# Optimization experiments

Measured on AMD Instinct MI355X. Metric: run time of the kernel, lower is better.

## Reference

```python
import jax, jax.numpy as jnp
import numpy as np

H = 12  # num_heads

def setup_inputs() -> dict:
    key = jax.random.key(0)
    ks = jax.random.split(key, 6)
    B, L, D = 2, 2048, 768
    x = jax.random.normal(ks[0], (B, L, D), dtype=jnp.float32)
    token_sizes = jax.random.uniform(ks[1], (B, L), dtype=jnp.float32)
    attn_mask = jnp.triu(jnp.ones((L, L), dtype=bool), k=1)
    key_padding_mask = jnp.zeros((B, L), dtype=bool)
    qkv_w = jax.random.normal(ks[2], (3 * D, D), dtype=jnp.float32) * (D ** -0.5)
    qkv_b = jax.random.normal(ks[3], (3 * D,), dtype=jnp.float32) * 0.02
    proj_w = jax.random.normal(ks[4], (D, D), dtype=jnp.float32) * (D ** -0.5)
    proj_b = jax.random.normal(ks[5], (D,), dtype=jnp.float32) * 0.02
    return {"x": x, "token_sizes": token_sizes, "attn_mask": attn_mask,
            "key_padding_mask": key_padding_mask, "qkv_w": qkv_w, "qkv_b": qkv_b,
            "proj_w": proj_w, "proj_b": proj_b}

def reference(x, token_sizes, attn_mask, key_padding_mask, qkv_w, qkv_b, proj_w, proj_b):
    B, L, D = x.shape
    hd = D // H
    scale = hd ** -0.5
    qkv = (x @ qkv_w.T + qkv_b).reshape(B, L, 3, H, hd)
    qkv = jnp.transpose(qkv, (2, 0, 3, 1, 4))  # [3, B, H, L, hd]
    q, k, v = qkv[0], qkv[1], qkv[2]
    logits = jnp.einsum('bhqd,bhkd->bhqk', q, k) * scale  # [B,H,L,L]
    neg = jnp.finfo(logits.dtype).min
    logits = jnp.where(attn_mask[None, None, :, :], neg, logits)
    logits = jnp.where(key_padding_mask[:, None, None, :], neg, logits)
    logits = logits + jnp.log(jnp.clip(token_sizes, 1e-8))[:, None, None, :]
    attn = jax.nn.softmax(logits, axis=-1)
    out = jnp.einsum('bhqk,bhkd->bhqd', attn, v)
    out = jnp.transpose(out, (0, 2, 1, 3)).reshape(B, L, D)
    out = out @ proj_w.T + proj_b
    k_merge = k.mean(axis=1)  # [B, L, hd]
    return (out, k_merge)
```

## Files before the change

### kernel.cpp

```cpp
#include <hip/hip_runtime.h>
#include <hip/hip_bf16.h>

typedef unsigned short u16;
typedef __bf16 bf16x8 __attribute__((ext_vector_type(8)));
typedef float f32x4 __attribute__((ext_vector_type(4)));

#define QSCALE (0.125f * 1.44269504088896340736f)

__device__ __forceinline__ u16 f2bf(float f) {
    __hip_bfloat16 h = __float2bfloat16(f);
    return __builtin_bit_cast(u16, h);
}
__device__ __forceinline__ float bf2f(u16 u) {
    unsigned int x = ((unsigned int)u) << 16;
    return __builtin_bit_cast(float, x);
}
__device__ __forceinline__ bf16x8 ld_bf8(const u16* p) {
    uint4 u = *reinterpret_cast<const uint4*>(p);
    return __builtin_bit_cast(bf16x8, u);
}
__device__ __forceinline__ bf16x8 pack8f(f32x4 a, f32x4 b) {
    union { bf16x8 v; u16 u[8]; } r;
    #pragma unroll
    for (int i = 0; i < 4; i++) { r.u[i] = f2bf(a[i]); r.u[4+i] = f2bf(b[i]); }
    return r.v;
}
__device__ __forceinline__ bf16x8 pack8u(ushort4 a, ushort4 b) {
    union { bf16x8 v; ushort4 u[2]; } r;
    r.u[0] = a; r.u[1] = b;
    return r.v;
}

#define GLOAD_LDS16(g, l) __builtin_amdgcn_global_load_lds( \
    (const __attribute__((address_space(1))) unsigned int*)(g), \
    (__attribute__((address_space(3))) unsigned int*)(l), 16, 0, 0)

__global__ __launch_bounds__(256) void prep_kernel(
    const float* __restrict__ x, const float* __restrict__ qkvw,
    const float* __restrict__ projw, const float* __restrict__ ts,
    const unsigned char* __restrict__ kpm,
    u16* __restrict__ Xb, u16* __restrict__ Wq, u16* __restrict__ Wp,
    float* __restrict__ tsw, int* __restrict__ qcount)
{
    int i = blockIdx.x * 256 + threadIdx.x;
    if (i == 0) *qcount = 0;
    const int XC4 = 4096 * 768 / 4;
    const int WQ4 = 2304 * 768 / 4;
    const int WP4 = 768 * 768 / 4;
    const float* src = nullptr; u16* dst = nullptr;
    if (i < XC4) { src = x; dst = Xb; }
    else {
        i -= XC4;
        if (i < WQ4) { src = qkvw; dst = Wq; }
        else {
            i -= WQ4;
            if (i < WP4) { src = projw; dst = Wp; }
            else {
                i -= WP4;
                if (i < 1024) {
                    float4 t = *(const float4*)(ts + i*4);
                    uchar4 k = *(const uchar4*)(kpm + i*4);
                    float4 r;
                    r.x = k.x ? 0.f : fmaxf(t.x, 1e-8f);
                    r.y = k.y ? 0.f : fmaxf(t.y, 1e-8f);
                    r.z = k.z ? 0.f : fmaxf(t.z, 1e-8f);
                    r.w = k.w ? 0.f : fmaxf(t.w, 1e-8f);
                    *(float4*)(tsw + i*4) = r;
                }
                return;
            }
        }
    }
    float4 v = *(const float4*)(src + i*4);
    ushort4 o;
    o.x = f2bf(v.x); o.y = f2bf(v.y); o.z = f2bf(v.z); o.w = f2bf(v.w);
    *(ushort4*)(dst + i*4) = o;
}

template<int EPI>
__global__ __launch_bounds__(256) void gemm_bt(
    const u16* __restrict__ A, const u16* __restrict__ Bm,
    const float* __restrict__ bias,
    u16* __restrict__ Qb, u16* __restrict__ Kb, u16* __restrict__ Vt,
    float* __restrict__ outp)
{
    __shared__ u16 As[2][128 * 32];
    __shared__ u16 Bs[2][128 * 32];
    const int K = 768;
    const int tid = threadIdx.x;
    const int m0 = blockIdx.y * 128;
    const int n0 = blockIdx.x * 128;
    const int w = tid >> 6, lane = tid & 63;
    const int wr = (w >> 1) * 64, wc = (w & 1) * 64;
    const int g = lane >> 4, l16 = lane & 15;

    const int srow = lane >> 2;
    const int scol = (lane & 3) * 8;
    const u16* gA0 = A  + (size_t)(m0 + w*32      + srow) * K + scol;
    const u16* gA1 = A  + (size_t)(m0 + w*32 + 16 + srow) * K + scol;
    const u16* gB0 = Bm + (size_t)(n0 + w*32      + srow) * K + scol;
    const u16* gB1 = Bm + (size_t)(n0 + w*32 + 16 + srow) * K + scol;

#define GSTAGE(buf, kk) do { \
    GLOAD_LDS16(gA0 + (kk), &As[buf][(w*32     ) * 32]); \
    GLOAD_LDS16(gA1 + (kk), &As[buf][(w*32 + 16) * 32]); \
    GLOAD_LDS16(gB0 + (kk), &Bs[buf][(w*32     ) * 32]); \
    GLOAD_LDS16(gB1 + (kk), &Bs[buf][(w*32 + 16) * 32]); } while (0)

    f32x4 acc[4][4] = {};
    GSTAGE(0, 0);
    __syncthreads();
    for (int k0 = 0; k0 < K; k0 += 32) {
        const int cur = (k0 >> 5) & 1;
        if (k0 + 32 < K) GSTAGE(cur ^ 1, k0 + 32);
        bf16x8 af[4], bfr[4];
        #pragma unroll
        for (int i = 0; i < 4; i++) af[i]  = ld_bf8(&As[cur][(wr + i*16 + l16)*32 + g*8]);
        #pragma unroll
        for (int j = 0; j < 4; j++) bfr[j] = ld_bf8(&Bs[cur][(wc + j*16 + l16)*32 + g*8]);
        #pragma unroll
        for (int i = 0; i < 4; i++)
            #pragma unroll
            for (int j = 0; j < 4; j++)
                acc[i][j] = __builtin_amdgcn_mfma_f32_16x16x32_bf16(af[i], bfr[j], acc[i][j], 0, 0, 0);
        __syncthreads();
    }
#undef GSTAGE

    #pragma unroll
    for (int j = 0; j < 4; j++) {
        const int n = n0 + wc + j*16 + l16;
        const float bs = bias[n];
        #pragma unroll
        for (int i = 0; i < 4; i++) {
            #pragma unroll
            for (int r = 0; r < 4; r++) {
                const int m = m0 + wr + i*16 + g*4 + r;
                float v = acc[i][j][r] + bs;
                if (EPI == 0) {
                    int b = m >> 11, l = m & 2047;
                    unsigned int which = (unsigned int)n / 768u;
                    int rem = n - (int)which * 768;
                    int h = rem >> 6, d = rem & 63;
                    int bh = b * 12 + h;
                    if (which == 0)      Qb[((size_t)bh*2048 + l)*64 + d] = f2bf(v * QSCALE);
                    else if (which == 1) Kb[((size_t)bh*2048 + l)*64 + d] = f2bf(v);
                    else                 Vt[((size_t)bh*64 + d)*2048 + l] = f2bf(v);
                } else {
                    outp[(size_t)m * 768 + n] = v;
                }
            }
        }
    }
}

__global__ __launch_bounds__(256, 2) void attn_kernel(
    const u16* __restrict__ Q, const u16* __restrict__ Kb,
    const u16* __restrict__ Vt, const float* __restrict__ tsw,
    u16* __restrict__ O, int* __restrict__ qcount)
{
    __shared__ u16 Ks[2][64 * 64];
    __shared__ u16 Vs[2][64 * 64];
    __shared__ int s_item;
    const int tid = threadIdx.x;
    const int w = tid >> 6, lane = tid & 63;
    const int g = lane >> 4, l16 = lane & 15;
    const int sw = l16 & 7;
    const int srow = lane >> 3;
    const int sslot = (lane & 7) ^ srow;

    bf16x8 ones;
    { union { bf16x8 v; u16 u[8]; } t;
      #pragma unroll
      for (int i = 0; i < 8; i++) t.u[i] = 0x3F80;
      ones = t.v; }

    for (;;) {
        if (tid == 0) s_item = atomicAdd(qcount, 1);
        __syncthreads();
        const int item = s_item;
        if (item >= 768) return;
        const int qt = 31 - (item / 24);
        const int bh = item - (item / 24) * 24;
        const int b = bh / 12, h = bh - b * 12;
        const int q0 = qt * 64 + w * 16;
        const int nkt = qt + 1;

        const u16* Qp = Q + ((size_t)bh * 2048 + q0) * 64;
        const u16* Kp = Kb + (size_t)bh * 2048 * 64;
        const u16* Vp = Vt + (size_t)bh * 64 * 2048;
        const float* tw = tsw + b * 2048;

        const u16* gK0 = Kp + (size_t)(w*16 +     srow) * 64   + sslot * 8;
        const u16* gK1 = Kp + (size_t)(w*16 + 8 + srow) * 64   + sslot * 8;
        const u16* gV0 = Vp + (size_t)(w*16 +     srow) * 2048 + sslot * 8;
        const u16* gV1 = Vp + (size_t)(w*16 + 8 + srow) * 2048 + sslot * 8;

#define ASTAGE(buf, kk) do { \
    GLOAD_LDS16(gK0 + (size_t)(kk) * 64, &Ks[buf][(w*16    ) * 64]); \
    GLOAD_LDS16(gK1 + (size_t)(kk) * 64, &Ks[buf][(w*16 + 8) * 64]); \
    GLOAD_LDS16(gV0 + (kk),              &Vs[buf][(w*16    ) * 64]); \
    GLOAD_LDS16(gV1 + (kk),              &Vs[buf][(w*16 + 8) * 64]); } while (0)

        const bf16x8 qf0 = ld_bf8(Qp + l16 * 64 + g * 8);
        const bf16x8 qf1 = ld_bf8(Qp + l16 * 64 + 32 + g * 8);

        f32x4 o[4] = {};
        f32x4 lpacc = {};
        float m = -1e30f;
        const int qmy = q0 + l16;

        ASTAGE(0, 0);
        __syncthreads();

        for (int kt = 0; kt < nkt; kt++) {
            const int cur = kt & 1;
            const int k0 = kt * 64;
            if (kt + 1 < nkt) ASTAGE(cur ^ 1, k0 + 64);

            f32x4 twv[4];
            #pragma unroll
            for (int t = 0; t < 4; t++)
                twv[t] = *(const f32x4*)(tw + k0 + t*16 + 4*g);

            const int ko0 = 8 * (g ^ sw);
            f32x4 s[4];
            #pragma unroll
            for (int t = 0; t < 4; t++) {
                const u16* kb = &Ks[cur][(t*16 + l16) * 64];
                bf16x8 kf0 = ld_bf8(kb + ko0);
                bf16x8 kf1 = ld_bf8(kb + (ko0 ^ 32));
                f32x4 z = {};
                z = __builtin_amdgcn_mfma_f32_16x16x32_bf16(kf0, qf0, z, 0, 0, 0);
                z = __builtin_amdgcn_mfma_f32_16x16x32_bf16(kf1, qf1, z, 0, 0, 0);
                s[t] = z;
            }
            if (kt == qt) {
                #pragma unroll
                for (int t = 0; t < 4; t++)
                    #pragma unroll
                    for (int r = 0; r < 4; r++) {
                        const int key = k0 + t*16 + 4*g + r;
                        if (key > qmy) s[t][r] = -1e30f;
                    }
            }
            float pmax = -1e30f;
            #pragma unroll
            for (int t = 0; t < 4; t++)
                #pragma unroll
                for (int r = 0; r < 4; r++)
                    pmax = fmaxf(pmax, s[t][r]);
            pmax = fmaxf(pmax, __shfl_xor(pmax, 16));
            pmax = fmaxf(pmax, __shfl_xor(pmax, 32));
            if (!__all(pmax <= m + 8.f)) {
                const float mn = fmaxf(m, pmax);
                const float sc = __builtin_amdgcn_exp2f(m - mn);
                m = mn;
                #pragma unroll
                for (int r = 0; r < 4; r++) {
                    const float scr = __shfl(sc, (lane & 48) + 4*g + r);
                    o[0][r] *= scr; o[1][r] *= scr; o[2][r] *= scr; o[3][r] *= scr;
                    lpacc[r] *= scr;
                }
            }
            #pragma unroll
            for (int t = 0; t < 4; t++)
                #pragma unroll
                for (int r = 0; r < 4; r++)
                    s[t][r] = __builtin_amdgcn_exp2f(s[t][r] - m) * twv[t][r];
            const bf16x8 pa01 = pack8f(s[0], s[1]);
            const bf16x8 pa23 = pack8f(s[2], s[3]);
            lpacc = __builtin_amdgcn_mfma_f32_16x16x32_bf16(pa01, ones, lpacc, 0, 0, 0);
            lpacc = __builtin_amdgcn_mfma_f32_16x16x32_bf16(pa23, ones, lpacc, 0, 0, 0);
            const int gh = g >> 1, gl = 4 * (g & 1);
            #pragma unroll
            for (int j = 0; j < 4; j++) {
                const u16* vb = &Vs[cur][(j*16 + l16) * 64];
                ushort4 va0 = *(const ushort4*)(vb + (((0 + gh) ^ sw) << 3) + gl);
                ushort4 va1 = *(const ushort4*)(vb + (((2 + gh) ^ sw) << 3) + gl);
                ushort4 va2 = *(const ushort4*)(vb + (((4 + gh) ^ sw) << 3) + gl);
                ushort4 va3 = *(const ushort4*)(vb + (((6 + gh) ^ sw) << 3) + gl);
                o[j] = __builtin_amdgcn_mfma_f32_16x16x32_bf16(pa01, pack8u(va0, va1), o[j], 0, 0, 0);
                o[j] = __builtin_amdgcn_mfma_f32_16x16x32_bf16(pa23, pack8u(va2, va3), o[j], 0, 0, 0);
            }
            __syncthreads();
        }
#undef ASTAGE

        float rlr[4];
        #pragma unroll
        for (int r = 0; r < 4; r++) rlr[r] = 1.f / lpacc[r];
        #pragma unroll
        for (int j = 0; j < 4; j++)
            #pragma unroll
            for (int r = 0; r < 4; r++) {
                const int q = q0 + 4*g + r;
                O[((size_t)b*2048 + q)*768 + h*64 + j*16 + l16] = f2bf(o[j][r] * rlr[r]);
            }
    }
}

__global__ __launch_bounds__(256) void kmerge_kernel(
    const u16* __restrict__ Kb, float* __restrict__ out)
{
    const int idx = blockIdx.x * 256 + threadIdx.x;
    const int d4 = (idx & 15) * 4;
    const int l = (idx >> 4) & 2047;
    const int b = idx >> 15;
    float4 acc = {0.f, 0.f, 0.f, 0.f};
    #pragma unroll
    for (int h = 0; h < 12; h++) {
        ushort4 v = *(const ushort4*)&Kb[(((size_t)(b*12 + h))*2048 + l)*64 + d4];
        acc.x += bf2f(v.x); acc.y += bf2f(v.y);
        acc.z += bf2f(v.z); acc.w += bf2f(v.w);
    }
    const float s = 1.f / 12.f;
    float4 r = {acc.x * s, acc.y * s, acc.z * s, acc.w * s};
    *(float4*)&out[(((size_t)b*2048 + l))*64 + d4] = r;
}

extern "C" void kernel_launch(void* const* d_in, const int* in_sizes, int n_in,
                              void* d_out, int out_size, void* d_ws, size_t ws_size,
                              hipStream_t stream)
{
    const float* x     = (const float*)d_in[0];
    const float* ts    = (const float*)d_in[1];
    const unsigned char* kpm = (const unsigned char*)d_in[3];
    const float* qkvw  = (const float*)d_in[4];
    const float* qkvb  = (const float*)d_in[5];
    const float* projw = (const float*)d_in[6];
    const float* projb = (const float*)d_in[7];
    float* out = (float*)d_out;

    char* ws = (char*)d_ws;
    u16* Xb = (u16*)ws;  ws += (size_t)4096 * 768 * 2;
    u16* Wq = (u16*)ws;  ws += (size_t)2304 * 768 * 2;
    u16* Wp = (u16*)ws;  ws += (size_t)768 * 768 * 2;
    u16* Qb = (u16*)ws;  ws += (size_t)24 * 2048 * 64 * 2;
    u16* Kb = (u16*)ws;  ws += (size_t)24 * 2048 * 64 * 2;
    u16* Vt = (u16*)ws;  ws += (size_t)24 * 2048 * 64 * 2;
    u16* Ob = (u16*)ws;  ws += (size_t)4096 * 768 * 2;
    float* tsw = (float*)ws;  ws += (size_t)2 * 2048 * 4;
    int* qcount = (int*)ws;

    const int prep4 = (4096*768 + 2304*768 + 768*768) / 4 + 1024;
    prep_kernel<<<(prep4 + 255) / 256, 256, 0, stream>>>(
        x, qkvw, projw, ts, kpm, Xb, Wq, Wp, tsw, qcount);

    gemm_bt<0><<<dim3(18, 32), 256, 0, stream>>>(Xb, Wq, qkvb, Qb, Kb, Vt, nullptr);

    attn_kernel<<<dim3(640), 256, 0, stream>>>(Qb, Kb, Vt, tsw, Ob, qcount);

    kmerge_kernel<<<(2*2048*16) / 256, 256, 0, stream>>>(Kb, out + 3145728);

    gemm_bt<1><<<dim3(6, 32), 256, 0, stream>>>(Ob, Wp, projb, nullptr, nullptr, nullptr, out);
}
```

Baseline: 118.8 us.

## Fold token-size weights into V and row-sum MFMA, swizzle GEMM blocks, hoist LDS loads

Token-size weights are now multiplied into V in the QKV GEMM epilogue. The softmax denominator uses a bf16 weight vector as the MFMA B operand, which removes the per-element weight multiply and the fp32 weight loads in the attention inner loop. GEMM workgroup indices are remapped in groups of eight to improve L2 locality. K and V fragments are loaded from LDS before the score MFMAs so the loads have more time to land, and the attention grid drops from 640 to 512 persistent blocks. The risks are bf16 rounding of the weights in both V and the denominator, and higher register pressure from hoisting the fragments.

```diff
diff --git a/kernel.cpp b/kernel.cpp
--- a/kernel.cpp
+++ b/kernel.cpp
@@ -40,7 +40,7 @@
     const float* __restrict__ projw, const float* __restrict__ ts,
     const unsigned char* __restrict__ kpm,
     u16* __restrict__ Xb, u16* __restrict__ Wq, u16* __restrict__ Wp,
-    float* __restrict__ tsw, int* __restrict__ qcount)
+    float* __restrict__ tsw, u16* __restrict__ tbf, int* __restrict__ qcount)
 {
     int i = blockIdx.x * 256 + threadIdx.x;
     if (i == 0) *qcount = 0;
@@ -66,6 +66,10 @@
                     r.z = k.z ? 0.f : fmaxf(t.z, 1e-8f);
                     r.w = k.w ? 0.f : fmaxf(t.w, 1e-8f);
                     *(float4*)(tsw + i*4) = r;
+                    ushort4 o;
+                    o.x = f2bf(r.x); o.y = f2bf(r.y);
+                    o.z = f2bf(r.z); o.w = f2bf(r.w);
+                    *(ushort4*)(tbf + i*4) = o;
                 }
                 return;
             }
@@ -80,7 +84,7 @@
 template<int EPI>
 __global__ __launch_bounds__(256) void gemm_bt(
     const u16* __restrict__ A, const u16* __restrict__ Bm,
-    const float* __restrict__ bias,
+    const float* __restrict__ bias, const float* __restrict__ tsw,
     u16* __restrict__ Qb, u16* __restrict__ Kb, u16* __restrict__ Vt,
     float* __restrict__ outp)
 {
@@ -88,8 +92,12 @@
     __shared__ u16 Bs[2][128 * 32];
     const int K = 768;
     const int tid = threadIdx.x;
-    const int m0 = blockIdx.y * 128;
-    const int n0 = blockIdx.x * 128;
+    const int nwg = gridDim.x * gridDim.y;
+    const int flat = blockIdx.y * gridDim.x + blockIdx.x;
+    const int per = nwg >> 3;
+    const int swz = (flat & 7) * per + (flat >> 3);
+    const int m0 = (swz / gridDim.x) * 128;
+    const int n0 = (swz % gridDim.x) * 128;
     const int w = tid >> 6, lane = tid & 63;
     const int wr = (w >> 1) * 64, wc = (w & 1) * 64;
     const int g = lane >> 4, l16 = lane & 15;
@@ -145,7 +153,7 @@
                     int bh = b * 12 + h;
                     if (which == 0)      Qb[((size_t)bh*2048 + l)*64 + d] = f2bf(v * QSCALE);
                     else if (which == 1) Kb[((size_t)bh*2048 + l)*64 + d] = f2bf(v);
-                    else                 Vt[((size_t)bh*64 + d)*2048 + l] = f2bf(v);
+                    else                 Vt[((size_t)bh*64 + d)*2048 + l] = f2bf(v * tsw[b*2048 + l]);
                 } else {
                     outp[(size_t)m * 768 + n] = v;
                 }
@@ -156,7 +164,7 @@
 
 __global__ __launch_bounds__(256, 2) void attn_kernel(
     const u16* __restrict__ Q, const u16* __restrict__ Kb,
-    const u16* __restrict__ Vt, const float* __restrict__ tsw,
+    const u16* __restrict__ Vt, const u16* __restrict__ tbf,
     u16* __restrict__ O, int* __restrict__ qcount)
 {
     __shared__ u16 Ks[2][64 * 64];
@@ -168,12 +176,6 @@
     const int sw = l16 & 7;
     const int srow = lane >> 3;
     const int sslot = (lane & 7) ^ srow;
-
-    bf16x8 ones;
-    { union { bf16x8 v; u16 u[8]; } t;
-      #pragma unroll
-      for (int i = 0; i < 8; i++) t.u[i] = 0x3F80;
-      ones = t.v; }
 
     for (;;) {
         if (tid == 0) s_item = atomicAdd(qcount, 1);
@@ -189,7 +191,7 @@
         const u16* Qp = Q + ((size_t)bh * 2048 + q0) * 64;
         const u16* Kp = Kb + (size_t)bh * 2048 * 64;
         const u16* Vp = Vt + (size_t)bh * 64 * 2048;
-        const float* tw = tsw + b * 2048;
+        const u16* tb = tbf + b * 2048;
 
         const u16* gK0 = Kp + (size_t)(w*16 +     srow) * 64   + sslot * 8;
         const u16* gK1 = Kp + (size_t)(w*16 + 8 + srow) * 64   + sslot * 8;
@@ -216,23 +218,40 @@
         for (int kt = 0; kt < nkt; kt++) {
             const int cur = kt & 1;
             const int k0 = kt * 64;
+
+            const u16* tp = tb + k0 + 4*g;
+            ushort4 t0 = *(const ushort4*)(tp);
+            ushort4 t1 = *(const ushort4*)(tp + 16);
+            ushort4 t2 = *(const ushort4*)(tp + 32);
+            ushort4 t3 = *(const ushort4*)(tp + 48);
+
             if (kt + 1 < nkt) ASTAGE(cur ^ 1, k0 + 64);
 
-            f32x4 twv[4];
-            #pragma unroll
-            for (int t = 0; t < 4; t++)
-                twv[t] = *(const f32x4*)(tw + k0 + t*16 + 4*g);
-
             const int ko0 = 8 * (g ^ sw);
-            f32x4 s[4];
+            bf16x8 kf[4][2];
             #pragma unroll
             for (int t = 0; t < 4; t++) {
                 const u16* kb = &Ks[cur][(t*16 + l16) * 64];
-                bf16x8 kf0 = ld_bf8(kb + ko0);
-                bf16x8 kf1 = ld_bf8(kb + (ko0 ^ 32));
+                kf[t][0] = ld_bf8(kb + ko0);
+                kf[t][1] = ld_bf8(kb + (ko0 ^ 32));
+            }
+            const int gh = g >> 1, gl = 4 * (g & 1);
+            ushort4 va[4][4];
+            #pragma unroll
+            for (int j = 0; j < 4; j++) {
+                const u16* vb = &Vs[cur][(j*16 + l16) * 64];
+                va[j][0] = *(const ushort4*)(vb + (((0 + gh) ^ sw) << 3) + gl);
+                va[j][1] = *(const ushort4*)(vb + (((2 + gh) ^ sw) << 3) + gl);
+                va[j][2] = *(const ushort4*)(vb + (((4 + gh) ^ sw) << 3) + gl);
+                va[j][3] = *(const ushort4*)(vb + (((6 + gh) ^ sw) << 3) + gl);
+            }
+
+            f32x4 s[4];
+            #pragma unroll
+            for (int t = 0; t < 4; t++) {
                 f32x4 z = {};
-                z = __builtin_amdgcn_mfma_f32_16x16x32_bf16(kf0, qf0, z, 0, 0, 0);
-                z = __builtin_amdgcn_mfma_f32_16x16x32_bf16(kf1, qf1, z, 0, 0, 0);
+                z = __builtin_amdgcn_mfma_f32_16x16x32_bf16(kf[t][0], qf0, z, 0, 0, 0);
+                z = __builtin_amdgcn_mfma_f32_16x16x32_bf16(kf[t][1], qf1, z, 0, 0, 0);
                 s[t] = z;
             }
             if (kt == qt) {
@@ -267,21 +286,15 @@
             for (int t = 0; t < 4; t++)
                 #pragma unroll
                 for (int r = 0; r < 4; r++)
-                    s[t][r] = __builtin_amdgcn_exp2f(s[t][r] - m) * twv[t][r];
+                    s[t][r] = __builtin_amdgcn_exp2f(s[t][r] - m);
             const bf16x8 pa01 = pack8f(s[0], s[1]);
             const bf16x8 pa23 = pack8f(s[2], s[3]);
-            lpacc = __builtin_amdgcn_mfma_f32_16x16x32_bf16(pa01, ones, lpacc, 0, 0, 0);
-            lpacc = __builtin_amdgcn_mfma_f32_16x16x32_bf16(pa23, ones, lpacc, 0, 0, 0);
-            const int gh = g >> 1, gl = 4 * (g & 1);
+            lpacc = __builtin_amdgcn_mfma_f32_16x16x32_bf16(pa01, pack8u(t0, t1), lpacc, 0, 0, 0);
+            lpacc = __builtin_amdgcn_mfma_f32_16x16x32_bf16(pa23, pack8u(t2, t3), lpacc, 0, 0, 0);
             #pragma unroll
             for (int j = 0; j < 4; j++) {
-                const u16* vb = &Vs[cur][(j*16 + l16) * 64];
-                ushort4 va0 = *(const ushort4*)(vb + (((0 + gh) ^ sw) << 3) + gl);
-                ushort4 va1 = *(const ushort4*)(vb + (((2 + gh) ^ sw) << 3) + gl);
-                ushort4 va2 = *(const ushort4*)(vb + (((4 + gh) ^ sw) << 3) + gl);
-                ushort4 va3 = *(const ushort4*)(vb + (((6 + gh) ^ sw) << 3) + gl);
-                o[j] = __builtin_amdgcn_mfma_f32_16x16x32_bf16(pa01, pack8u(va0, va1), o[j], 0, 0, 0);
-                o[j] = __builtin_amdgcn_mfma_f32_16x16x32_bf16(pa23, pack8u(va2, va3), o[j], 0, 0, 0);
+                o[j] = __builtin_amdgcn_mfma_f32_16x16x32_bf16(pa01, pack8u(va[j][0], va[j][1]), o[j], 0, 0, 0);
+                o[j] = __builtin_amdgcn_mfma_f32_16x16x32_bf16(pa23, pack8u(va[j][2], va[j][3]), o[j], 0, 0, 0);
             }
             __syncthreads();
         }
@@ -341,17 +354,18 @@
     u16* Vt = (u16*)ws;  ws += (size_t)24 * 2048 * 64 * 2;
     u16* Ob = (u16*)ws;  ws += (size_t)4096 * 768 * 2;
     float* tsw = (float*)ws;  ws += (size_t)2 * 2048 * 4;
+    u16* tbf = (u16*)ws;  ws += (size_t)2 * 2048 * 2;
     int* qcount = (int*)ws;
 
     const int prep4 = (4096*768 + 2304*768 + 768*768) / 4 + 1024;
     prep_kernel<<<(prep4 + 255) / 256, 256, 0, stream>>>(
-        x, qkvw, projw, ts, kpm, Xb, Wq, Wp, tsw, qcount);
-
-    gemm_bt<0><<<dim3(18, 32), 256, 0, stream>>>(Xb, Wq, qkvb, Qb, Kb, Vt, nullptr);
-
-    attn_kernel<<<dim3(640), 256, 0, stream>>>(Qb, Kb, Vt, tsw, Ob, qcount);
+        x, qkvw, projw, ts, kpm, Xb, Wq, Wp, tsw, tbf, qcount);
+
+    gemm_bt<0><<<dim3(18, 32), 256, 0, stream>>>(Xb, Wq, qkvb, tsw, Qb, Kb, Vt, nullptr);
+
+    attn_kernel<<<dim3(512), 256, 0, stream>>>(Qb, Kb, Vt, tbf, Ob, qcount);
 
     kmerge_kernel<<<(2*2048*16) / 256, 256, 0, stream>>>(Kb, out + 3145728);
 
-    gemm_bt<1><<<dim3(6, 32), 256, 0, stream>>>(Ob, Wp, projb, nullptr, nullptr, nullptr, out);
-}
+    gemm_bt<1><<<dim3(6, 32), 256, 0, stream>>>(Ob, Wp, projb, nullptr, nullptr, nullptr, nullptr, out);
+}
```

Measured after the change: 110.7 us. 1.07x faster.
